# Kernel tuning notes

Measured on AMD Instinct MI355X. Metric: run time of the kernel, lower is better.

The kernel has to match this reference:

```python
import jax, jax.numpy as jnp
import numpy as np

N_NODES = 20000
N_EDGES = 640000
D = 128


def setup_inputs() -> dict:
    key = jax.random.key(0)
    ks = jax.random.split(key, 8)
    scale = 1.0 / np.sqrt(D)
    x = jax.random.normal(ks[0], (N_NODES, D), dtype=jnp.float32)
    edge_index = jax.random.randint(ks[1], (2, N_EDGES), 0, N_NODES, dtype=jnp.int64)
    W1_rel = jax.random.normal(ks[2], (D, D), dtype=jnp.float32) * scale
    b1_rel = jnp.zeros((D,), dtype=jnp.float32)
    W1_root = jax.random.normal(ks[3], (D, D), dtype=jnp.float32) * scale
    W2_rel = jax.random.normal(ks[4], (D, D), dtype=jnp.float32) * scale
    b2_rel = jnp.zeros((D,), dtype=jnp.float32)
    W2_root = jax.random.normal(ks[5], (D, D), dtype=jnp.float32) * scale
    return {"x": x, "edge_index": edge_index,
            "W1_rel": W1_rel, "b1_rel": b1_rel, "W1_root": W1_root,
            "W2_rel": W2_rel, "b2_rel": b2_rel, "W2_root": W2_root}


def _graph_conv(x, src, dst, W_rel, b_rel, W_root):
    # sum-aggregate neighbor features: gather from src, scatter-add to dst
    agg = jax.ops.segment_sum(x[src], dst, num_segments=N_NODES)  # [N, D]
    # PyG GraphConv: lin_rel(agg) (with bias) + lin_root(x) (no bias)
    return agg @ W_rel + b_rel + x @ W_root


def reference(x, edge_index, W1_rel, b1_rel, W1_root, W2_rel, b2_rel, W2_root):
    src, dst = edge_index[0], edge_index[1]  # messages flow src (j) -> dst (i)
    h = jax.nn.relu(_graph_conv(x, src, dst, W1_rel, b1_rel, W1_root))
    out = _graph_conv(h, src, dst, W2_rel, b2_rel, W2_root)  # final ReLU stripped
    return out
```

## Files before the change

kernel.cpp:

```cpp
#include <hip/hip_runtime.h>

#define N_NODES 20000
#define N_EDGES 640000
#define D 128
#define CAP 128

typedef __attribute__((ext_vector_type(8))) short bf16x8;
typedef __attribute__((ext_vector_type(4))) float f32x4;

__device__ __forceinline__ short f2bf(float f) {
    union { float f; unsigned u; } un; un.f = f;
    unsigned r = un.u + 0x7fff + ((un.u >> 16) & 1);
    return (short)(r >> 16);
}
__device__ __forceinline__ float bflo(unsigned u) { return __uint_as_float(u << 16); }
__device__ __forceinline__ float bfhi(unsigned u) { return __uint_as_float(u & 0xffff0000u); }

__global__ __launch_bounds__(256) void prep_kernel(
    const float* __restrict__ x,
    const int* __restrict__ src, const int* __restrict__ dst,
    const float* __restrict__ W1_rel, const float* __restrict__ W1_root,
    const float* __restrict__ W2_rel, const float* __restrict__ W2_root,
    int* __restrict__ cnt, unsigned short* __restrict__ buckets,
    short* __restrict__ xb, short* __restrict__ wpk1, short* __restrict__ wpk2)
{
    const int b = blockIdx.x;
    const int tid = threadIdx.x;
    if (b < 625) {
        int e4 = b * 256 + tid;
        int4 s4 = ((const int4*)src)[e4];
        int4 d4 = ((const int4*)dst)[e4];
#pragma unroll
        for (int q = 0; q < 4; q++) {
            int d = (&d4.x)[q];
            int s = (&s4.x)[q];
            int p = atomicAdd(&cnt[d], 1);
            if (p < CAP) buckets[(d << 7) + p] = (unsigned short)s;
        }
    } else if (b < 3125) {
        int i = (b - 625) * 256 + tid;
        float4 v = ((const float4*)x)[i];
        ushort4 o;
        o.x = (unsigned short)f2bf(v.x);
        o.y = (unsigned short)f2bf(v.y);
        o.z = (unsigned short)f2bf(v.z);
        o.w = (unsigned short)f2bf(v.w);
        ((ushort4*)xb)[i] = o;
    } else {
        int pb  = b - 3125;
        int job = pb >> 4;
        int idx = (pb & 15) * 256 + tid;
        const float* Wrel  = job ? W2_rel  : W1_rel;
        const float* Wroot = job ? W2_root : W1_root;
        short* Wpk = job ? wpk2 : wpk1;
        int lane = idx & 63;
        int ct   = (idx >> 6) & 7;
        int t    = idx >> 9;
        const float* W = (t < 4) ? Wrel : Wroot;
        int k0  = (t & 3) * 32 + (lane >> 4) * 8;
        int col = ct * 16 + (lane & 15);
        bf16x8 pk;
#pragma unroll
        for (int j = 0; j < 8; j++)
            pk[j] = f2bf(W[(size_t)(k0 + j) * D + col]);
        ((bf16x8*)Wpk)[idx] = pk;
    }
}

template <bool RELU, bool OUT_BF16>
__global__ __launch_bounds__(512) void layer_kernel(
    const short* __restrict__ xin,
    const int* __restrict__ cnt,
    const unsigned short* __restrict__ buckets,
    const short* __restrict__ Wpk,
    const float* __restrict__ brel,
    void* __restrict__ outp)
{
    __shared__ short sAgg[16][136];

    const int tid  = threadIdx.x;
    const int row0 = blockIdx.x * 16;

    {
        const int hw   = tid >> 5;
        const int lane = tid & 31;
        const int node = row0 + hw;
        int n = cnt[node];
        n = (n > CAP) ? CAP : n;
        uint2 idxpk = *(const uint2*)(buckets + (node << 7) + lane * 4);

        float4 acc = make_float4(0.f, 0.f, 0.f, 0.f);
        int i = 0;
        for (; i + 8 <= n; i += 8) {
            int baseLane = i >> 2;
            uint2 u[8];
#pragma unroll
            for (int q = 0; q < 8; q++) {
                unsigned word = __shfl((q & 2) ? idxpk.y : idxpk.x,
                                       baseLane + (q >> 2), 32);
                unsigned sidx = (q & 1) ? (word >> 16) : (word & 0xffffu);
                u[q] = *(const uint2*)(xin + (size_t)sidx * D + lane * 4);
            }
#pragma unroll
            for (int q = 0; q < 8; q++) {
                acc.x += bflo(u[q].x); acc.y += bfhi(u[q].x);
                acc.z += bflo(u[q].y); acc.w += bfhi(u[q].y);
            }
        }
        for (; i < n; i++) {
            unsigned word = __shfl((i & 2) ? idxpk.y : idxpk.x, i >> 2, 32);
            unsigned sidx = (i & 1) ? (word >> 16) : (word & 0xffffu);
            uint2 u0 = *(const uint2*)(xin + (size_t)sidx * D + lane * 4);
            acc.x += bflo(u0.x); acc.y += bfhi(u0.x);
            acc.z += bflo(u0.y); acc.w += bfhi(u0.y);
        }
        ushort4 o;
        o.x = (unsigned short)f2bf(acc.x);
        o.y = (unsigned short)f2bf(acc.y);
        o.z = (unsigned short)f2bf(acc.z);
        o.w = (unsigned short)f2bf(acc.w);
        *(ushort4*)&sAgg[hw][lane * 4] = o;
    }
    __syncthreads();

    const int wave = tid >> 6;
    const int lane = tid & 63;
    const int quad = lane >> 4;
    const int l16  = lane & 15;

    f32x4 acc = (f32x4){0.f, 0.f, 0.f, 0.f};
    const short* arow_x = xin + (size_t)(row0 + l16) * D + quad * 8;
    const bf16x8* wb = (const bf16x8*)Wpk + lane;

#pragma unroll
    for (int t = 0; t < 8; t++) {
        bf16x8 a;
        if (t < 4)
            a = *(const bf16x8*)&sAgg[l16][(t & 3) * 32 + quad * 8];
        else
            a = *(const bf16x8*)(arow_x + (t & 3) * 32);
        bf16x8 bfr = wb[(t * 8 + wave) * 64];
        acc = __builtin_amdgcn_mfma_f32_16x16x32_bf16(a, bfr, acc, 0, 0, 0);
    }

    const int col  = wave * 16 + l16;
    const int orow = row0 + quad * 4;
    const float bias = brel[col];
#pragma unroll
    for (int r = 0; r < 4; r++) {
        float v = acc[r] + bias;
        if (RELU) v = fmaxf(v, 0.f);
        if (OUT_BF16)
            ((short*)outp)[(size_t)(orow + r) * D + col] = f2bf(v);
        else
            ((float*)outp)[(size_t)(orow + r) * D + col] = v;
    }
}

extern "C" void kernel_launch(void* const* d_in, const int* in_sizes, int n_in,
                              void* d_out, int out_size, void* d_ws, size_t ws_size,
                              hipStream_t stream) {
    const float* x       = (const float*)d_in[0];
    const int*   ei      = (const int*)  d_in[1];
    const float* W1_rel  = (const float*)d_in[2];
    const float* b1_rel  = (const float*)d_in[3];
    const float* W1_root = (const float*)d_in[4];
    const float* W2_rel  = (const float*)d_in[5];
    const float* b2_rel  = (const float*)d_in[6];
    const float* W2_root = (const float*)d_in[7];
    float* out = (float*)d_out;

    char* p = (char*)d_ws;
    short* xb   = (short*)p;  p += (size_t)N_NODES * D * 2;
    short* hb   = (short*)p;  p += (size_t)N_NODES * D * 2;
    short* wpk1 = (short*)p;  p += 65536;
    short* wpk2 = (short*)p;  p += 65536;
    int*   cnt  = (int*)p;    p += (size_t)N_NODES * 4;
    unsigned short* buckets = (unsigned short*)p;

    const int* src = ei;
    const int* dst = ei + N_EDGES;

    const int layerblocks = N_NODES / 16;

    hipMemsetAsync(cnt, 0, (size_t)N_NODES * sizeof(int), stream);
    prep_kernel<<<3157, 256, 0, stream>>>(
        x, src, dst, W1_rel, W1_root, W2_rel, W2_root,
        cnt, buckets, xb, wpk1, wpk2);

    layer_kernel<true, true><<<layerblocks, 512, 0, stream>>>(
        xb, cnt, buckets, wpk1, b1_rel, (void*)hb);

    layer_kernel<false, false><<<layerblocks, 512, 0, stream>>>(
        hb, cnt, buckets, wpk2, b2_rel, (void*)out);
}
```

Baseline: 160.0 us.

## Replace global-atomic edge bucketing with two-pass shared-memory binning

Edge bucketing by destination moves from one global atomicAdd per edge to two passes. First, each block bins its edges into shared memory by dst>>7 and appends each bin to a global bin with one atomic per bin. Second, a new kernel scatters each bin into per-node buckets using shared-memory atomics and writes the counts. This cuts global atomic traffic and contention but adds an extra kernel launch, an intermediate buffer round trip, and fixed capacities (LCAP, BINCAP) that could silently drop edges under skewed inputs.

```diff
diff --git a/kernel.cpp b/kernel.cpp
--- a/kernel.cpp
+++ b/kernel.cpp
@@ -4,6 +4,9 @@
 #define N_EDGES 640000
 #define D 128
 #define CAP 128
+#define NBINS 157
+#define LCAP 48
+#define BINCAP 5120
 
 typedef __attribute__((ext_vector_type(8))) short bf16x8;
 typedef __attribute__((ext_vector_type(4))) float f32x4;
@@ -16,29 +19,60 @@
 __device__ __forceinline__ float bflo(unsigned u) { return __uint_as_float(u << 16); }
 __device__ __forceinline__ float bfhi(unsigned u) { return __uint_as_float(u & 0xffff0000u); }
 
-__global__ __launch_bounds__(256) void prep_kernel(
+__global__ __launch_bounds__(256) void prep1_kernel(
     const float* __restrict__ x,
     const int* __restrict__ src, const int* __restrict__ dst,
     const float* __restrict__ W1_rel, const float* __restrict__ W1_root,
     const float* __restrict__ W2_rel, const float* __restrict__ W2_root,
-    int* __restrict__ cnt, unsigned short* __restrict__ buckets,
+    int* __restrict__ gbincnt, unsigned* __restrict__ gbins,
     short* __restrict__ xb, short* __restrict__ wpk1, short* __restrict__ wpk2)
 {
+    __shared__ unsigned lbin[NBINS * LCAP];
+    __shared__ int lbincnt[NBINS];
+
     const int b = blockIdx.x;
     const int tid = threadIdx.x;
-    if (b < 625) {
-        int e4 = b * 256 + tid;
-        int4 s4 = ((const int4*)src)[e4];
-        int4 d4 = ((const int4*)dst)[e4];
-#pragma unroll
-        for (int q = 0; q < 4; q++) {
-            int d = (&d4.x)[q];
-            int s = (&s4.x)[q];
-            int p = atomicAdd(&cnt[d], 1);
-            if (p < CAP) buckets[(d << 7) + p] = (unsigned short)s;
-        }
-    } else if (b < 3125) {
-        int i = (b - 625) * 256 + tid;
+
+    if (b < 313) {
+        for (int i = tid; i < NBINS; i += 256) lbincnt[i] = 0;
+        __syncthreads();
+
+        int base4 = (b * 256 + tid) * 2;
+#pragma unroll
+        for (int h = 0; h < 2; h++) {
+            int e4 = base4 + h;
+            if (e4 < N_EDGES / 4) {
+                int4 s4 = ((const int4*)src)[e4];
+                int4 d4 = ((const int4*)dst)[e4];
+#pragma unroll
+                for (int q = 0; q < 4; q++) {
+                    int d = (&d4.x)[q];
+                    int s = (&s4.x)[q];
+                    int bin = d >> 7;
+                    int lpos = atomicAdd(&lbincnt[bin], 1);
+                    if (lpos < LCAP)
+                        lbin[bin * LCAP + lpos] = ((unsigned)d << 16) | (unsigned)s;
+                }
+            }
+        }
+        __syncthreads();
+
+        const int wid = tid >> 6;
+        const int lane = tid & 63;
+        for (int b2 = wid; b2 < NBINS; b2 += 4) {
+            int lcnt = lbincnt[b2];
+            lcnt = (lcnt > LCAP) ? LCAP : lcnt;
+            int gbase = 0;
+            if (lane == 0 && lcnt > 0) gbase = atomicAdd(&gbincnt[b2], lcnt);
+            gbase = __shfl(gbase, 0, 64);
+            if (lane < lcnt) {
+                int gpos = gbase + lane;
+                if (gpos < BINCAP)
+                    gbins[b2 * BINCAP + gpos] = lbin[b2 * LCAP + lane];
+            }
+        }
+    } else if (b < 2813) {
+        int i = (b - 313) * 256 + tid;
         float4 v = ((const float4*)x)[i];
         ushort4 o;
         o.x = (unsigned short)f2bf(v.x);
@@ -47,7 +81,7 @@
         o.w = (unsigned short)f2bf(v.w);
         ((ushort4*)xb)[i] = o;
     } else {
-        int pb  = b - 3125;
+        int pb  = b - 2813;
         int job = pb >> 4;
         int idx = (pb & 15) * 256 + tid;
         const float* Wrel  = job ? W2_rel  : W1_rel;
@@ -67,6 +101,35 @@
     }
 }
 
+__global__ __launch_bounds__(256) void prep2_kernel(
+    const int* __restrict__ gbincnt, const unsigned* __restrict__ gbins,
+    int* __restrict__ cnt, unsigned short* __restrict__ buckets)
+{
+    __shared__ int lcur[128];
+    const int b = blockIdx.x;
+    const int tid = threadIdx.x;
+    if (tid < 128) lcur[tid] = 0;
+    __syncthreads();
+
+    int m = gbincnt[b];
+    m = (m > BINCAP) ? BINCAP : m;
+    const unsigned* bin = gbins + b * BINCAP;
+    for (int i = tid; i < m; i += 256) {
+        unsigned pk = bin[i];
+        int d = (int)(pk >> 16);
+        int s = (int)(pk & 0xffffu);
+        int pos = atomicAdd(&lcur[d & 127], 1);
+        if (pos < CAP) buckets[(d << 7) + pos] = (unsigned short)s;
+    }
+    __syncthreads();
+
+    int node = b * 128 + tid;
+    if (tid < 128 && node < N_NODES) {
+        int c = lcur[tid];
+        cnt[node] = (c > CAP) ? CAP : c;
+    }
+}
+
 template <bool RELU, bool OUT_BF16>
 __global__ __launch_bounds__(512) void layer_kernel(
     const short* __restrict__ xin,
@@ -177,16 +240,20 @@
     short* wpk2 = (short*)p;  p += 65536;
     int*   cnt  = (int*)p;    p += (size_t)N_NODES * 4;
     unsigned short* buckets = (unsigned short*)p;
+    p += (size_t)N_NODES * CAP * 2;
+    int* gbincnt = (int*)p;   p += 4096;
+    unsigned* gbins = (unsigned*)p;
 
     const int* src = ei;
     const int* dst = ei + N_EDGES;
 
     const int layerblocks = N_NODES / 16;
 
-    hipMemsetAsync(cnt, 0, (size_t)N_NODES * sizeof(int), stream);
-    prep_kernel<<<3157, 256, 0, stream>>>(
+    hipMemsetAsync(gbincnt, 0, 4096, stream);
+    prep1_kernel<<<2845, 256, 0, stream>>>(
         x, src, dst, W1_rel, W1_root, W2_rel, W2_root,
-        cnt, buckets, xb, wpk1, wpk2);
+        gbincnt, gbins, xb, wpk1, wpk2);
+    prep2_kernel<<<NBINS, 256, 0, stream>>>(gbincnt, gbins, cnt, buckets);
 
     layer_kernel<true, true><<<layerblocks, 512, 0, stream>>>(
         xb, cnt, buckets, wpk1, b1_rel, (void*)hb);
```

Result: slower. 364.8 us (+128.0%).

## Dynamically assign aggregation nodes to full waves via LDS atomic counter

Applied to the files above, without the earlier changes.

The gather-aggregation phase changes from a fixed half-wave per node (32 lanes, 4 bf16 per lane) to whole 64-lane waves that claim nodes one at a time from a shared atomic counter, each lane handling 2 bf16 features. This is meant to balance uneven node degrees across the 8 waves and cut the load imbalance a static mapping gives. In exchange each gathered row is read with narrower 4-byte loads, and an LDS atomic plus a shuffle is added per node, which may reduce memory-level parallelism.

```diff
diff --git a/kernel.cpp b/kernel.cpp
--- a/kernel.cpp
+++ b/kernel.cpp
@@ -77,54 +77,54 @@
     void* __restrict__ outp)
 {
     __shared__ short sAgg[16][136];
+    __shared__ int nextNode;
 
     const int tid  = threadIdx.x;
     const int row0 = blockIdx.x * 16;
+    const int lane = tid & 63;
 
-    {
-        const int hw   = tid >> 5;
-        const int lane = tid & 31;
-        const int node = row0 + hw;
+    if (tid == 0) nextNode = 0;
+    __syncthreads();
+
+    for (;;) {
+        int pos = 0;
+        if (lane == 0) pos = atomicAdd(&nextNode, 1);
+        pos = __shfl(pos, 0, 64);
+        if (pos >= 16) break;
+
+        const int node = row0 + pos;
         int n = cnt[node];
         n = (n > CAP) ? CAP : n;
-        uint2 idxpk = *(const uint2*)(buckets + (node << 7) + lane * 4);
+        unsigned idxw = *(const unsigned*)(buckets + (node << 7) + lane * 2);
+        const short* xbase = xin + lane * 2;
 
-        float4 acc = make_float4(0.f, 0.f, 0.f, 0.f);
+        float acx = 0.f, acy = 0.f;
         int i = 0;
         for (; i + 8 <= n; i += 8) {
-            int baseLane = i >> 2;
-            uint2 u[8];
+            unsigned u[8];
 #pragma unroll
             for (int q = 0; q < 8; q++) {
-                unsigned word = __shfl((q & 2) ? idxpk.y : idxpk.x,
-                                       baseLane + (q >> 2), 32);
-                unsigned sidx = (q & 1) ? (word >> 16) : (word & 0xffffu);
-                u[q] = *(const uint2*)(xin + (size_t)sidx * D + lane * 4);
+                int j = i + q;
+                unsigned w = __shfl(idxw, j >> 1, 64);
+                unsigned sidx = (j & 1) ? (w >> 16) : (w & 0xffffu);
+                u[q] = *(const unsigned*)(xbase + (size_t)sidx * D);
             }
 #pragma unroll
-            for (int q = 0; q < 8; q++) {
-                acc.x += bflo(u[q].x); acc.y += bfhi(u[q].x);
-                acc.z += bflo(u[q].y); acc.w += bfhi(u[q].y);
-            }
+            for (int q = 0; q < 8; q++) { acx += bflo(u[q]); acy += bfhi(u[q]); }
         }
         for (; i < n; i++) {
-            unsigned word = __shfl((i & 2) ? idxpk.y : idxpk.x, i >> 2, 32);
-            unsigned sidx = (i & 1) ? (word >> 16) : (word & 0xffffu);
-            uint2 u0 = *(const uint2*)(xin + (size_t)sidx * D + lane * 4);
-            acc.x += bflo(u0.x); acc.y += bfhi(u0.x);
-            acc.z += bflo(u0.y); acc.w += bfhi(u0.y);
+            unsigned w = __shfl(idxw, i >> 1, 64);
+            unsigned sidx = (i & 1) ? (w >> 16) : (w & 0xffffu);
+            unsigned u0 = *(const unsigned*)(xbase + (size_t)sidx * D);
+            acx += bflo(u0); acy += bfhi(u0);
         }
-        ushort4 o;
-        o.x = (unsigned short)f2bf(acc.x);
-        o.y = (unsigned short)f2bf(acc.y);
-        o.z = (unsigned short)f2bf(acc.z);
-        o.w = (unsigned short)f2bf(acc.w);
-        *(ushort4*)&sAgg[hw][lane * 4] = o;
+        unsigned pk = ((unsigned)(unsigned short)f2bf(acx))
+                    | (((unsigned)(unsigned short)f2bf(acy)) << 16);
+        *(unsigned*)&sAgg[pos][lane * 2] = pk;
     }
     __syncthreads();
 
     const int wave = tid >> 6;
-    const int lane = tid & 63;
     const int quad = lane >> 4;
     const int l16  = lane & 15;
 
```

After: 174.8 us. 9.2% more time.
